# Performance work log

Hardware: AMD Instinct MI355X
Metric: run time of the kernel (lower is better)

Reference implementation:

```python
import jax, jax.numpy as jnp
from jax import lax
import numpy as np

SEQ, BATCH, IN, HID = 512, 256, 248, 1024


def setup_inputs() -> dict:
    key = jax.random.key(0)
    ks = jax.random.split(key, 9)
    s_in = 1.0 / np.sqrt(HID)  # pytorch default init scale for RNN/Linear
    x = jax.random.normal(ks[0], (SEQ, BATCH, IN), dtype=jnp.float32)
    W_ih = jax.random.uniform(ks[1], (HID, IN), jnp.float32, -s_in, s_in)
    b_ih = jax.random.uniform(ks[2], (HID,), jnp.float32, -s_in, s_in)
    W_hh = jax.random.uniform(ks[3], (HID, HID), jnp.float32, -s_in, s_in)
    b_hh = jax.random.uniform(ks[4], (HID,), jnp.float32, -s_in, s_in)
    W_out = jax.random.uniform(ks[5], (1, HID), jnp.float32, -s_in, s_in)
    b_out = jax.random.uniform(ks[6], (1,), jnp.float32, -s_in, s_in)
    w_r = jax.random.uniform(ks[7], (1, 1), jnp.float32, -1.0, 1.0)
    b_r = jax.random.uniform(ks[8], (1,), jnp.float32, -1.0, 1.0)
    return {"x": x, "W_ih": W_ih, "b_ih": b_ih, "W_hh": W_hh, "b_hh": b_hh,
            "W_out": W_out, "b_out": b_out, "w_r": w_r, "b_r": b_r}


def reference(x, W_ih, b_ih, W_hh, b_hh, W_out, b_out, w_r, b_r):
    # x: (T, B, IN) time-major, like torch nn.RNN default.
    T, B, _ = x.shape
    H = W_hh.shape[0]
    # Precompute input projection for all timesteps: (T, B, H)
    xproj = jnp.einsum('tbi,hi->tbh', x, W_ih) + b_ih + b_hh

    def rnn_step(h, xp):
        h_new = jnp.tanh(xp + h @ W_hh.T)
        return h_new, h_new

    h0 = jnp.zeros((B, H), dtype=x.dtype)
    _, hs = lax.scan(rnn_step, h0, xproj)  # hs: (T, B, H)

    # Output logits for all timesteps: (T, B, 1)
    z = jnp.einsum('tbh,oh->tbo', hs, W_out) + b_out

    # o_0 = sigmoid(z_0); o_t = sigmoid(z_t + recurr(o_{t-1}))
    o0 = jax.nn.sigmoid(z[0])

    def out_step(o_prev, zt):
        o = jax.nn.sigmoid(zt + o_prev @ w_r.T + b_r)
        return o, o

    _, os = lax.scan(out_step, o0, z[1:])
    o_all = jnp.concatenate([o0[None], os], axis=0)  # (T, B, 1)
    return o_all[:, :, 0].T  # (B, T), matching oFinal
```

## Files before the change

kernel.cpp:

```cpp
#include <hip/hip_runtime.h>

#define T_SEQ 512
#define NB    256
#define NIN   248
#define NH    1024

typedef __attribute__((ext_vector_type(8))) short          short8;
typedef __attribute__((ext_vector_type(4))) float          f32x4;
typedef __attribute__((ext_vector_type(4))) unsigned int   uint4v;
typedef __attribute__((ext_vector_type(4))) float          float4v;
typedef unsigned long long u64;

#define AS_RELAXED __ATOMIC_RELAXED
#define AS_AGENT   __HIP_MEMORY_SCOPE_AGENT

__device__ __forceinline__ unsigned short f2bf(float f){
  unsigned int u = __float_as_uint(f);
  u += 0x7FFFu + ((u >> 16) & 1u);
  return (unsigned short)(u >> 16);
}

__device__ __forceinline__ float tanh_fast(float v){
  float e = __expf(2.0f * v);
  return 1.0f - 2.0f / (e + 1.0f);
}

__launch_bounds__(256, 1)
__global__ void rnn_scan_kernel(const float* __restrict__ x,
                                const float* __restrict__ W_ih,
                                const float* __restrict__ b_ih,
                                const float* __restrict__ W_hh,
                                const float* __restrict__ b_hh,
                                const float* __restrict__ W_out,
                                unsigned short* __restrict__ hbuf,
                                float* __restrict__ z,
                                unsigned int* __restrict__ bar)
{
  __shared__ alignas(16) unsigned short h_frag[2048 * 8];
  __shared__ alignas(16) unsigned short x_frag[512 * 8];
  __shared__ alignas(8)  unsigned short h_out[16 * 64];
  __shared__ float z_hist[T_SEQ * 16];

  const int tid    = threadIdx.x;
  const int wg     = blockIdx.x;
  const int r16    = wg & 15;
  const int bg     = (r16 & 7) * 2 + (r16 >> 3);
  const int jg     = wg >> 4;
  const int b_base = bg * 16;
  const int l      = tid & 63;
  const int wv     = tid >> 6;
  const int n      = l & 15;
  const int quad   = l >> 4;
  const int j      = jg * 64 + wv * 16 + n;

  unsigned short* h0 = hbuf;
  unsigned short* h1 = hbuf + (size_t)NB * NH;
  unsigned int* flags = bar + bg * 32;

  short8 whh[32];
  #pragma unroll
  for (int kt = 0; kt < 32; ++kt){
    const float* p = W_hh + (size_t)j * NH + kt * 32 + quad * 8;
    float4v a = *(const float4v*)p;
    float4v b = *(const float4v*)(p + 4);
    short8 v;
    v[0]=(short)f2bf(a[0]); v[1]=(short)f2bf(a[1]); v[2]=(short)f2bf(a[2]); v[3]=(short)f2bf(a[3]);
    v[4]=(short)f2bf(b[0]); v[5]=(short)f2bf(b[1]); v[6]=(short)f2bf(b[2]); v[7]=(short)f2bf(b[3]);
    whh[kt] = v;
  }
  short8 wih[8];
  #pragma unroll
  for (int kt = 0; kt < 8; ++kt){
    short8 v = {0,0,0,0,0,0,0,0};
    if (!(kt == 7 && quad == 3)){
      const float* p = W_ih + (size_t)j * NIN + kt * 32 + quad * 8;
      float4v a = *(const float4v*)p;
      float4v b = *(const float4v*)(p + 4);
      v[0]=(short)f2bf(a[0]); v[1]=(short)f2bf(a[1]); v[2]=(short)f2bf(a[2]); v[3]=(short)f2bf(a[3]);
      v[4]=(short)f2bf(b[0]); v[5]=(short)f2bf(b[1]); v[6]=(short)f2bf(b[2]); v[7]=(short)f2bf(b[3]);
    }
    wih[kt] = v;
  }
  const float bias  = b_ih[j] + b_hh[j];
  const float woutj = W_out[j];

  #pragma unroll
  for (int i = 0; i < 32; ++i) z_hist[tid + i * 256] = 0.f;
  {
    int r = tid >> 4, c = (tid & 15) * 4;
    __hip_atomic_store((u64*)&h0[(size_t)(b_base + r) * NH + jg * 64 + c],
                       0ull, AS_RELAXED, AS_AGENT);
    int tt = jg * 32 + (tid >> 3);
    int bb = (tid & 7) * 2;
    __hip_atomic_store(&z[(size_t)tt * NB + b_base + bb],     0.f, AS_RELAXED, AS_AGENT);
    __hip_atomic_store(&z[(size_t)tt * NB + b_base + bb + 1], 0.f, AS_RELAXED, AS_AGENT);
  }

  const int xslot_kt[2] = { tid >> 6, (tid + 256) >> 6 };
  const int xslot_l2[2] = { tid & 63, tid & 63 };
  float4v xr[2][2];
  bool    xvalid[2];
  #pragma unroll
  for (int i = 0; i < 2; ++i){
    int kt = xslot_kt[i], l2 = xslot_l2[i];
    int b = b_base + (l2 & 15), k = kt * 32 + (l2 >> 4) * 8;
    xvalid[i] = !(kt == 7 && (l2 >> 4) == 3);
    if (xvalid[i]){
      const float* p = x + ((size_t)0 * NB + b) * NIN + k;
      xr[i][0] = *(const float4v*)p;
      xr[i][1] = *(const float4v*)(p + 4);
    }
  }

  __syncthreads();
  if (tid == 0)
    __hip_atomic_store(&flags[jg], 1u, AS_RELAXED, AS_AGENT);

  for (int t = 0; t < T_SEQ; ++t){
    const unsigned short* hp = (t & 1) ? h1 : h0;
    unsigned short*       hn = (t & 1) ? h0 : h1;

    {
      const unsigned int tgt = (unsigned)(t + 1);
      const unsigned int* f = &flags[l & 15];
      while (__hip_atomic_load(f, AS_RELAXED, AS_AGENT) < tgt)
        __builtin_amdgcn_s_sleep(1);
    }

    u64 hw0[8], hw1[8];
    #pragma unroll
    for (int i = 0; i < 8; ++i){
      int slot = tid + i * 256;
      int kt = slot >> 6, l2 = slot & 63;
      int b = b_base + (l2 & 15), k = kt * 32 + (l2 >> 4) * 8;
      const u64* src = (const u64*)(hp + (size_t)b * NH + k);
      hw0[i] = __hip_atomic_load(src,     AS_RELAXED, AS_AGENT);
      hw1[i] = __hip_atomic_load(src + 1, AS_RELAXED, AS_AGENT);
    }
    #pragma unroll
    for (int i = 0; i < 2; ++i){
      int slot = tid + i * 256;
      uint4v v = {0u,0u,0u,0u};
      if (xvalid[i]){
        v[0] = (unsigned)f2bf(xr[i][0][0]) | ((unsigned)f2bf(xr[i][0][1]) << 16);
        v[1] = (unsigned)f2bf(xr[i][0][2]) | ((unsigned)f2bf(xr[i][0][3]) << 16);
        v[2] = (unsigned)f2bf(xr[i][1][0]) | ((unsigned)f2bf(xr[i][1][1]) << 16);
        v[3] = (unsigned)f2bf(xr[i][1][2]) | ((unsigned)f2bf(xr[i][1][3]) << 16);
      }
      *(uint4v*)&x_frag[slot * 8] = v;
    }
    #pragma unroll
    for (int i = 0; i < 8; ++i){
      u64* dst = (u64*)&h_frag[(tid + i * 256) * 8];
      dst[0] = hw0[i]; dst[1] = hw1[i];
    }
    __syncthreads();

    f32x4 a0 = {bias, bias, bias, bias};
    f32x4 a1 = {0.f, 0.f, 0.f, 0.f};
    f32x4 a2 = {0.f, 0.f, 0.f, 0.f};
    f32x4 a3 = {0.f, 0.f, 0.f, 0.f};
    #pragma unroll
    for (int kt = 0; kt < 32; kt += 4){
      short8 f0 = *(const short8*)&h_frag[((kt + 0) * 64 + l) * 8];
      short8 f1 = *(const short8*)&h_frag[((kt + 1) * 64 + l) * 8];
      short8 f2 = *(const short8*)&h_frag[((kt + 2) * 64 + l) * 8];
      short8 f3 = *(const short8*)&h_frag[((kt + 3) * 64 + l) * 8];
      a0 = __builtin_amdgcn_mfma_f32_16x16x32_bf16(f0, whh[kt + 0], a0, 0, 0, 0);
      a1 = __builtin_amdgcn_mfma_f32_16x16x32_bf16(f1, whh[kt + 1], a1, 0, 0, 0);
      a2 = __builtin_amdgcn_mfma_f32_16x16x32_bf16(f2, whh[kt + 2], a2, 0, 0, 0);
      a3 = __builtin_amdgcn_mfma_f32_16x16x32_bf16(f3, whh[kt + 3], a3, 0, 0, 0);
    }
    #pragma unroll
    for (int kt = 0; kt < 8; kt += 4){
      short8 f0 = *(const short8*)&x_frag[((kt + 0) * 64 + l) * 8];
      short8 f1 = *(const short8*)&x_frag[((kt + 1) * 64 + l) * 8];
      short8 f2 = *(const short8*)&x_frag[((kt + 2) * 64 + l) * 8];
      short8 f3 = *(const short8*)&x_frag[((kt + 3) * 64 + l) * 8];
      a0 = __builtin_amdgcn_mfma_f32_16x16x32_bf16(f0, wih[kt + 0], a0, 0, 0, 0);
      a1 = __builtin_amdgcn_mfma_f32_16x16x32_bf16(f1, wih[kt + 1], a1, 0, 0, 0);
      a2 = __builtin_amdgcn_mfma_f32_16x16x32_bf16(f2, wih[kt + 2], a2, 0, 0, 0);
      a3 = __builtin_amdgcn_mfma_f32_16x16x32_bf16(f3, wih[kt + 3], a3, 0, 0, 0);
    }

    {
      int tn = (t + 1 < T_SEQ) ? t + 1 : t;
      #pragma unroll
      for (int i = 0; i < 2; ++i){
        if (xvalid[i]){
          int kt = xslot_kt[i], l2 = xslot_l2[i];
          int b = b_base + (l2 & 15), k = kt * 32 + (l2 >> 4) * 8;
          const float* p = x + ((size_t)tn * NB + b) * NIN + k;
          xr[i][0] = *(const float4v*)p;
          xr[i][1] = *(const float4v*)(p + 4);
        }
      }
    }

    float hv[4];
    #pragma unroll
    for (int i = 0; i < 4; ++i){
      hv[i] = tanh_fast(a0[i] + a1[i] + a2[i] + a3[i]);
      h_out[(quad * 4 + i) * 64 + wv * 16 + n] = f2bf(hv[i]);
    }
    __syncthreads();

    {
      int r = tid >> 4, c = (tid & 15) * 4;
      u64 v = *(const u64*)&h_out[r * 64 + c];
      __hip_atomic_store((u64*)&hn[(size_t)(b_base + r) * NH + jg * 64 + c],
                         v, AS_RELAXED, AS_AGENT);
    }
    float sv[4];
    #pragma unroll
    for (int i = 0; i < 4; ++i) sv[i] = hv[i] * woutj;
    #pragma unroll
    for (int m = 1; m < 16; m <<= 1){
      #pragma unroll
      for (int i = 0; i < 4; ++i) sv[i] += __shfl_xor(sv[i], m, 64);
    }
    if (n == 0){
      #pragma unroll
      for (int i = 0; i < 4; ++i) atomicAdd(&z_hist[t * 16 + quad * 4 + i], sv[i]);
    }

    __syncthreads();
    if (tid == 0)
      __hip_atomic_store(&flags[jg], (unsigned)(t + 2), AS_RELAXED, AS_AGENT);
  }

  __syncthreads();
  #pragma unroll
  for (int i = 0; i < 32; ++i){
    int idx = tid + i * 256;
    int tt = idx >> 4, bb = idx & 15;
    atomicAdd(&z[(size_t)tt * NB + b_base + bb], z_hist[idx]);
  }
}

__global__ void out_scan_kernel(const float* __restrict__ z,
                                const float* __restrict__ b_out,
                                const float* __restrict__ w_r,
                                const float* __restrict__ b_r,
                                float* __restrict__ out)
{
  int b = threadIdx.x;
  float bo = b_out[0], wr = w_r[0], br = b_r[0];
  float o = 0.f;
  for (int t = 0; t < T_SEQ; ++t){
    float pre = z[(size_t)t * NB + b] + bo;
    if (t > 0) pre += wr * o + br;
    o = 1.0f / (1.0f + __expf(-pre));
    out[(size_t)b * T_SEQ + t] = o;
  }
}

extern "C" void kernel_launch(void* const* d_in, const int* in_sizes, int n_in,
                              void* d_out, int out_size, void* d_ws, size_t ws_size,
                              hipStream_t stream)
{
  (void)in_sizes; (void)n_in; (void)out_size; (void)ws_size;
  const float* x     = (const float*)d_in[0];
  const float* W_ih  = (const float*)d_in[1];
  const float* b_ih  = (const float*)d_in[2];
  const float* W_hh  = (const float*)d_in[3];
  const float* b_hh  = (const float*)d_in[4];
  const float* W_out = (const float*)d_in[5];
  const float* b_out = (const float*)d_in[6];
  const float* w_r   = (const float*)d_in[7];
  const float* b_r   = (const float*)d_in[8];
  float* out = (float*)d_out;

  unsigned short* hbuf = (unsigned short*)d_ws;
  float* z = (float*)((char*)d_ws + 2 * (size_t)NB * NH * sizeof(unsigned short));
  unsigned int* bar = (unsigned int*)((char*)d_ws
                        + 2 * (size_t)NB * NH * sizeof(unsigned short)
                        + (size_t)T_SEQ * NB * sizeof(float));

  hipMemsetAsync(bar, 0, 16 * 32 * sizeof(unsigned int), stream);

  rnn_scan_kernel<<<dim3(256), dim3(256), 0, stream>>>(
      x, W_ih, b_ih, W_hh, b_hh, W_out, hbuf, z, bar);

  out_scan_kernel<<<dim3(1), dim3(256), 0, stream>>>(z, b_out, w_r, b_r, out);
}
```

Measured before the change: 2.250 ms.

## Use per-wave flags and split LDS staging to shorten the per-step critical path

Replaces the per-workgroup flag, which needed a block-wide barrier before signalling, with per-wavefront flags. Each wave now publishes its own 16 hidden columns and raises its flag as soon as its global store completes. The h staging into LDS is split in two halves so MFMAs on the first half can start while the second half is written. A speculative flag read at the end of each step lets waves skip the spin loop when neighbours are already done. The x prefetch is moved after the flag store. This adds more flags to poll (64 per batch group) and relies on hand-placed waitcnt/sched barriers for correctness.

```diff
diff --git a/kernel.cpp b/kernel.cpp
--- a/kernel.cpp
+++ b/kernel.cpp
@@ -19,10 +19,18 @@
   u += 0x7FFFu + ((u >> 16) & 1u);
   return (unsigned short)(u >> 16);
 }
-
+__device__ __forceinline__ unsigned pk2(float lo, float hi){
+  return (unsigned)f2bf(lo) | ((unsigned)f2bf(hi) << 16);
+}
 __device__ __forceinline__ float tanh_fast(float v){
   float e = __expf(2.0f * v);
   return 1.0f - 2.0f / (e + 1.0f);
+}
+
+__device__ __forceinline__ void barrier_lds(){
+  asm volatile("s_waitcnt lgkmcnt(0)" ::: "memory");
+  __builtin_amdgcn_s_barrier();
+  __builtin_amdgcn_sched_barrier(0);
 }
 
 __launch_bounds__(256, 1)
@@ -38,7 +46,7 @@
 {
   __shared__ alignas(16) unsigned short h_frag[2048 * 8];
   __shared__ alignas(16) unsigned short x_frag[512 * 8];
-  __shared__ alignas(8)  unsigned short h_out[16 * 64];
+  __shared__ alignas(8)  unsigned short h_out[4 * 256];
   __shared__ float z_hist[T_SEQ * 16];
 
   const int tid    = threadIdx.x;
@@ -55,7 +63,7 @@
 
   unsigned short* h0 = hbuf;
   unsigned short* h1 = hbuf + (size_t)NB * NH;
-  unsigned int* flags = bar + bg * 32;
+  unsigned int* flags = bar + bg * 64;
 
   short8 whh[32];
   #pragma unroll
@@ -95,6 +103,9 @@
     __hip_atomic_store(&z[(size_t)tt * NB + b_base + bb],     0.f, AS_RELAXED, AS_AGENT);
     __hip_atomic_store(&z[(size_t)tt * NB + b_base + bb + 1], 0.f, AS_RELAXED, AS_AGENT);
   }
+  asm volatile("s_waitcnt vmcnt(0)" ::: "memory");
+  if (l == 0)
+    __hip_atomic_store(&flags[jg * 4 + wv], 1u, AS_RELAXED, AS_AGENT);
 
   const int xslot_kt[2] = { tid >> 6, (tid + 256) >> 6 };
   const int xslot_l2[2] = { tid & 63, tid & 63 };
@@ -112,104 +123,124 @@
     }
   }
 
-  __syncthreads();
-  if (tid == 0)
-    __hip_atomic_store(&flags[jg], 1u, AS_RELAXED, AS_AGENT);
+  unsigned spec = 0;
 
   for (int t = 0; t < T_SEQ; ++t){
     const unsigned short* hp = (t & 1) ? h1 : h0;
     unsigned short*       hn = (t & 1) ? h0 : h1;
-
-    {
-      const unsigned int tgt = (unsigned)(t + 1);
-      const unsigned int* f = &flags[l & 15];
-      while (__hip_atomic_load(f, AS_RELAXED, AS_AGENT) < tgt)
+    const int tn = (t + 1 < T_SEQ) ? t + 1 : t;
+
+    if (!__all((int)(spec >= (unsigned)(t + 1)))){
+      unsigned v;
+      do {
         __builtin_amdgcn_s_sleep(1);
-    }
+        v = __hip_atomic_load(&flags[l], AS_RELAXED, AS_AGENT);
+      } while (!__all((int)(v >= (unsigned)(t + 1))));
+    }
+    __builtin_amdgcn_sched_barrier(0);
 
     u64 hw0[8], hw1[8];
     #pragma unroll
     for (int i = 0; i < 8; ++i){
       int slot = tid + i * 256;
       int kt = slot >> 6, l2 = slot & 63;
-      int b = b_base + (l2 & 15), k = kt * 32 + (l2 >> 4) * 8;
-      const u64* src = (const u64*)(hp + (size_t)b * NH + k);
+      const u64* src = (const u64*)(hp
+          + (size_t)(b_base + (l2 & 15)) * NH + kt * 32 + (l2 >> 4) * 8);
       hw0[i] = __hip_atomic_load(src,     AS_RELAXED, AS_AGENT);
       hw1[i] = __hip_atomic_load(src + 1, AS_RELAXED, AS_AGENT);
     }
     #pragma unroll
     for (int i = 0; i < 2; ++i){
-      int slot = tid + i * 256;
       uint4v v = {0u,0u,0u,0u};
       if (xvalid[i]){
-        v[0] = (unsigned)f2bf(xr[i][0][0]) | ((unsigned)f2bf(xr[i][0][1]) << 16);
-        v[1] = (unsigned)f2bf(xr[i][0][2]) | ((unsigned)f2bf(xr[i][0][3]) << 16);
-        v[2] = (unsigned)f2bf(xr[i][1][0]) | ((unsigned)f2bf(xr[i][1][1]) << 16);
-        v[3] = (unsigned)f2bf(xr[i][1][2]) | ((unsigned)f2bf(xr[i][1][3]) << 16);
+        v[0] = pk2(xr[i][0][0], xr[i][0][1]);
+        v[1] = pk2(xr[i][0][2], xr[i][0][3]);
+        v[2] = pk2(xr[i][1][0], xr[i][1][1]);
+        v[3] = pk2(xr[i][1][2], xr[i][1][3]);
       }
-      *(uint4v*)&x_frag[slot * 8] = v;
-    }
-    #pragma unroll
-    for (int i = 0; i < 8; ++i){
+      *(uint4v*)&x_frag[(tid + i * 256) * 8] = v;
+    }
+    #pragma unroll
+    for (int i = 0; i < 4; ++i){
       u64* dst = (u64*)&h_frag[(tid + i * 256) * 8];
       dst[0] = hw0[i]; dst[1] = hw1[i];
     }
-    __syncthreads();
+    barrier_lds();
 
     f32x4 a0 = {bias, bias, bias, bias};
     f32x4 a1 = {0.f, 0.f, 0.f, 0.f};
     f32x4 a2 = {0.f, 0.f, 0.f, 0.f};
     f32x4 a3 = {0.f, 0.f, 0.f, 0.f};
     #pragma unroll
-    for (int kt = 0; kt < 32; kt += 4){
-      short8 f0 = *(const short8*)&h_frag[((kt + 0) * 64 + l) * 8];
-      short8 f1 = *(const short8*)&h_frag[((kt + 1) * 64 + l) * 8];
-      short8 f2 = *(const short8*)&h_frag[((kt + 2) * 64 + l) * 8];
-      short8 f3 = *(const short8*)&h_frag[((kt + 3) * 64 + l) * 8];
-      a0 = __builtin_amdgcn_mfma_f32_16x16x32_bf16(f0, whh[kt + 0], a0, 0, 0, 0);
-      a1 = __builtin_amdgcn_mfma_f32_16x16x32_bf16(f1, whh[kt + 1], a1, 0, 0, 0);
-      a2 = __builtin_amdgcn_mfma_f32_16x16x32_bf16(f2, whh[kt + 2], a2, 0, 0, 0);
-      a3 = __builtin_amdgcn_mfma_f32_16x16x32_bf16(f3, whh[kt + 3], a3, 0, 0, 0);
+    for (int kt = 0; kt < 16; kt += 4){
+      short8 q0 = *(const short8*)&h_frag[((kt + 0) * 64 + l) * 8];
+      short8 q1 = *(const short8*)&h_frag[((kt + 1) * 64 + l) * 8];
+      short8 q2 = *(const short8*)&h_frag[((kt + 2) * 64 + l) * 8];
+      short8 q3 = *(const short8*)&h_frag[((kt + 3) * 64 + l) * 8];
+      a0 = __builtin_amdgcn_mfma_f32_16x16x32_bf16(q0, whh[kt + 0], a0, 0, 0, 0);
+      a1 = __builtin_amdgcn_mfma_f32_16x16x32_bf16(q1, whh[kt + 1], a1, 0, 0, 0);
+      a2 = __builtin_amdgcn_mfma_f32_16x16x32_bf16(q2, whh[kt + 2], a2, 0, 0, 0);
+      a3 = __builtin_amdgcn_mfma_f32_16x16x32_bf16(q3, whh[kt + 3], a3, 0, 0, 0);
+    }
+    __builtin_amdgcn_sched_barrier(0);
+
+    #pragma unroll
+    for (int i = 4; i < 8; ++i){
+      u64* dst = (u64*)&h_frag[(tid + i * 256) * 8];
+      dst[0] = hw0[i]; dst[1] = hw1[i];
+    }
+    barrier_lds();
+
+    #pragma unroll
+    for (int kt = 16; kt < 32; kt += 4){
+      short8 q0 = *(const short8*)&h_frag[((kt + 0) * 64 + l) * 8];
+      short8 q1 = *(const short8*)&h_frag[((kt + 1) * 64 + l) * 8];
+      short8 q2 = *(const short8*)&h_frag[((kt + 2) * 64 + l) * 8];
+      short8 q3 = *(const short8*)&h_frag[((kt + 3) * 64 + l) * 8];
+      a0 = __builtin_amdgcn_mfma_f32_16x16x32_bf16(q0, whh[kt + 0], a0, 0, 0, 0);
+      a1 = __builtin_amdgcn_mfma_f32_16x16x32_bf16(q1, whh[kt + 1], a1, 0, 0, 0);
+      a2 = __builtin_amdgcn_mfma_f32_16x16x32_bf16(q2, whh[kt + 2], a2, 0, 0, 0);
+      a3 = __builtin_amdgcn_mfma_f32_16x16x32_bf16(q3, whh[kt + 3], a3, 0, 0, 0);
     }
     #pragma unroll
     for (int kt = 0; kt < 8; kt += 4){
-      short8 f0 = *(const short8*)&x_frag[((kt + 0) * 64 + l) * 8];
-      short8 f1 = *(const short8*)&x_frag[((kt + 1) * 64 + l) * 8];
-      short8 f2 = *(const short8*)&x_frag[((kt + 2) * 64 + l) * 8];
-      short8 f3 = *(const short8*)&x_frag[((kt + 3) * 64 + l) * 8];
-      a0 = __builtin_amdgcn_mfma_f32_16x16x32_bf16(f0, wih[kt + 0], a0, 0, 0, 0);
-      a1 = __builtin_amdgcn_mfma_f32_16x16x32_bf16(f1, wih[kt + 1], a1, 0, 0, 0);
-      a2 = __builtin_amdgcn_mfma_f32_16x16x32_bf16(f2, wih[kt + 2], a2, 0, 0, 0);
-      a3 = __builtin_amdgcn_mfma_f32_16x16x32_bf16(f3, wih[kt + 3], a3, 0, 0, 0);
-    }
-
-    {
-      int tn = (t + 1 < T_SEQ) ? t + 1 : t;
-      #pragma unroll
-      for (int i = 0; i < 2; ++i){
-        if (xvalid[i]){
-          int kt = xslot_kt[i], l2 = xslot_l2[i];
-          int b = b_base + (l2 & 15), k = kt * 32 + (l2 >> 4) * 8;
-          const float* p = x + ((size_t)tn * NB + b) * NIN + k;
-          xr[i][0] = *(const float4v*)p;
-          xr[i][1] = *(const float4v*)(p + 4);
-        }
-      }
+      short8 q0 = *(const short8*)&x_frag[((kt + 0) * 64 + l) * 8];
+      short8 q1 = *(const short8*)&x_frag[((kt + 1) * 64 + l) * 8];
+      short8 q2 = *(const short8*)&x_frag[((kt + 2) * 64 + l) * 8];
+      short8 q3 = *(const short8*)&x_frag[((kt + 3) * 64 + l) * 8];
+      a0 = __builtin_amdgcn_mfma_f32_16x16x32_bf16(q0, wih[kt + 0], a0, 0, 0, 0);
+      a1 = __builtin_amdgcn_mfma_f32_16x16x32_bf16(q1, wih[kt + 1], a1, 0, 0, 0);
+      a2 = __builtin_amdgcn_mfma_f32_16x16x32_bf16(q2, wih[kt + 2], a2, 0, 0, 0);
+      a3 = __builtin_amdgcn_mfma_f32_16x16x32_bf16(q3, wih[kt + 3], a3, 0, 0, 0);
     }
 
     float hv[4];
     #pragma unroll
     for (int i = 0; i < 4; ++i){
       hv[i] = tanh_fast(a0[i] + a1[i] + a2[i] + a3[i]);
-      h_out[(quad * 4 + i) * 64 + wv * 16 + n] = f2bf(hv[i]);
-    }
-    __syncthreads();
-
+      h_out[wv * 256 + (quad * 4 + i) * 16 + n] = f2bf(hv[i]);
+    }
     {
-      int r = tid >> 4, c = (tid & 15) * 4;
-      u64 v = *(const u64*)&h_out[r * 64 + c];
-      __hip_atomic_store((u64*)&hn[(size_t)(b_base + r) * NH + jg * 64 + c],
-                         v, AS_RELAXED, AS_AGENT);
+      int r = l >> 2, c = (l & 3) * 4;
+      u64 v = *(const u64*)&h_out[wv * 256 + r * 16 + c];
+      __hip_atomic_store((u64*)&hn[(size_t)(b_base + r) * NH
+                         + jg * 64 + wv * 16 + c], v, AS_RELAXED, AS_AGENT);
+    }
+    asm volatile("s_waitcnt vmcnt(0)" ::: "memory");
+    if (l == 0)
+      __hip_atomic_store(&flags[jg * 4 + wv], (unsigned)(t + 2),
+                         AS_RELAXED, AS_AGENT);
+    __builtin_amdgcn_sched_barrier(0);
+
+    #pragma unroll
+    for (int i = 0; i < 2; ++i){
+      if (xvalid[i]){
+        int kt = xslot_kt[i], l2 = xslot_l2[i];
+        int b = b_base + (l2 & 15), k = kt * 32 + (l2 >> 4) * 8;
+        const float* p = x + ((size_t)tn * NB + b) * NIN + k;
+        xr[i][0] = *(const float4v*)p;
+        xr[i][1] = *(const float4v*)(p + 4);
+      }
     }
     float sv[4];
     #pragma unroll
@@ -223,10 +254,7 @@
       #pragma unroll
       for (int i = 0; i < 4; ++i) atomicAdd(&z_hist[t * 16 + quad * 4 + i], sv[i]);
     }
-
-    __syncthreads();
-    if (tid == 0)
-      __hip_atomic_store(&flags[jg], (unsigned)(t + 2), AS_RELAXED, AS_AGENT);
+    spec = __hip_atomic_load(&flags[l], AS_RELAXED, AS_AGENT);
   }
 
   __syncthreads();
@@ -277,7 +305,7 @@
                         + 2 * (size_t)NB * NH * sizeof(unsigned short)
                         + (size_t)T_SEQ * NB * sizeof(float));
 
-  hipMemsetAsync(bar, 0, 16 * 32 * sizeof(unsigned int), stream);
+  hipMemsetAsync(bar, 0, 16 * 64 * sizeof(unsigned int), stream);
 
   rnn_scan_kernel<<<dim3(256), dim3(256), 0, stream>>>(
       x, W_ih, b_ih, W_hh, b_hh, W_out, hbuf, z, bar);
```

Measured after the change: 2.436 ms. 1.08x slower.
